# Performance work log

Measured on AMD Instinct MI355X. Metric: run time of the kernel, lower is better.

## Reference

```python
import jax, jax.numpy as jnp
import numpy as np

EPS = 1e-6

def setup_inputs() -> dict:
    key = jax.random.key(0)
    k1, k2 = jax.random.split(key)
    B, M, N, D = 4, 4096, 4096, 64
    input_features = jax.random.uniform(k1, (B, N, D), dtype=jnp.float32)
    input_associations = jax.random.uniform(k2, (B, M, N), dtype=jnp.float32)
    return {"input_features": input_features, "input_associations": input_associations}

def reference(input_features, input_associations):
    # feat: [B, N, D], assoc: [B, M, N]
    assoc_safe = input_associations + EPS
    assoc_norm = assoc_safe / jnp.sum(assoc_safe, axis=2, keepdims=True)  # normalize over N
    # weighted aggregation == batched matmul: [B,M,N] @ [B,N,D] -> [B,M,D]
    return jnp.einsum('bmn,bnd->bmd', assoc_norm, input_features)
```

## Files before the change

### kernel.cpp

```cpp
#include <hip/hip_runtime.h>

constexpr int Bn = 4;
constexpr int Mm = 4096;
constexpr int Nn = 4096;
constexpr int Dd = 64;
#define EPS_VAL 1e-6f

typedef __attribute__((ext_vector_type(8))) short short8_t;
typedef __attribute__((ext_vector_type(4))) float floatx4;

__device__ __forceinline__ unsigned short f32_to_bf16_rne(float x) {
    unsigned u = __float_as_uint(x);
    unsigned r = u + 0x7FFFu + ((u >> 16) & 1u);
    return (unsigned short)(r >> 16);
}

__global__ __launch_bounds__(256) void transpose_feat_kernel(
    const float* __restrict__ feat, unsigned short* __restrict__ ft)
{
    __shared__ unsigned short tile[64][66];
    const int b  = blockIdx.x >> 6;
    const int n0 = (blockIdx.x & 63) * 64;
    const int t  = threadIdx.x;
    const int row = t >> 2;
    const int seg = t & 3;

    const float* src = feat + ((size_t)(b * Nn + n0 + row)) * Dd + seg * 16;
    #pragma unroll
    for (int v = 0; v < 4; ++v) {
        float4 f = ((const float4*)src)[v];
        tile[row][seg * 16 + v * 4 + 0] = f32_to_bf16_rne(f.x);
        tile[row][seg * 16 + v * 4 + 1] = f32_to_bf16_rne(f.y);
        tile[row][seg * 16 + v * 4 + 2] = f32_to_bf16_rne(f.z);
        tile[row][seg * 16 + v * 4 + 3] = f32_to_bf16_rne(f.w);
    }
    __syncthreads();

    const int d    = row;
    const int nseg = seg;
    short8_t v0, v1;
    #pragma unroll
    for (int i = 0; i < 8; ++i) v0[i] = (short)tile[nseg * 16 + i][d];
    #pragma unroll
    for (int i = 0; i < 8; ++i) v1[i] = (short)tile[nseg * 16 + 8 + i][d];

    unsigned short* dst = ft + ((size_t)(b * Dd + d)) * Nn + n0 + nseg * 16;
    *(short8_t*)(dst)     = v0;
    *(short8_t*)(dst + 8) = v1;
}

__global__ __launch_bounds__(256, 1) void agg_kernel(
    const float* __restrict__ assoc, const unsigned short* __restrict__ ft,
    float* __restrict__ out)
{
    const int b  = blockIdx.x >> 6;
    const int mt = blockIdx.x & 63;
    const int w  = threadIdx.x >> 6;
    const int l  = threadIdx.x & 63;
    const int q  = l >> 4;
    const int mi = l & 15;
    const int m0 = mt * 64 + w * 16;

    const float* aptr = assoc + ((size_t)b * Mm + (size_t)(m0 + mi)) * Nn + q * 8;
    const unsigned short* fptr = ft + (size_t)b * Dd * Nn + (size_t)mi * Nn + q * 8;

    floatx4 acc0 = {0.f, 0.f, 0.f, 0.f};
    floatx4 acc1 = acc0, acc2 = acc0, acc3 = acc0;
    float s0 = 0.f, s1 = 0.f;

    #pragma unroll 4
    for (int k0 = 0; k0 < Nn; k0 += 32) {
        float4 alo = *(const float4*)(aptr + k0);
        float4 ahi = *(const float4*)(aptr + k0 + 4);
        float av[8] = {alo.x, alo.y, alo.z, alo.w, ahi.x, ahi.y, ahi.z, ahi.w};

        short8_t afrag;
        #pragma unroll
        for (int j = 0; j < 8; ++j) {
            unsigned short h = f32_to_bf16_rne(av[j] + EPS_VAL);
            afrag[j] = (short)h;
            float hv = __uint_as_float(((unsigned)h) << 16);
            if (j & 1) s1 += hv; else s0 += hv;
        }

        short8_t bf0 = *(const short8_t*)(fptr + k0);
        short8_t bf1 = *(const short8_t*)(fptr + k0 + 16 * Nn);
        short8_t bf2 = *(const short8_t*)(fptr + k0 + 32 * Nn);
        short8_t bf3 = *(const short8_t*)(fptr + k0 + 48 * Nn);

        acc0 = __builtin_amdgcn_mfma_f32_16x16x32_bf16(afrag, bf0, acc0, 0, 0, 0);
        acc1 = __builtin_amdgcn_mfma_f32_16x16x32_bf16(afrag, bf1, acc1, 0, 0, 0);
        acc2 = __builtin_amdgcn_mfma_f32_16x16x32_bf16(afrag, bf2, acc2, 0, 0, 0);
        acc3 = __builtin_amdgcn_mfma_f32_16x16x32_bf16(afrag, bf3, acc3, 0, 0, 0);
    }

    float s = s0 + s1;
    s += __shfl_xor(s, 16);
    s += __shfl_xor(s, 32);

    #pragma unroll
    for (int r = 0; r < 4; ++r) {
        float Sr  = __shfl(s, q * 4 + r);
        float inv = 1.0f / Sr;
        size_t base = ((size_t)b * Mm + (size_t)(m0 + q * 4 + r)) * Dd + mi;
        out[base +  0] = acc0[r] * inv;
        out[base + 16] = acc1[r] * inv;
        out[base + 32] = acc2[r] * inv;
        out[base + 48] = acc3[r] * inv;
    }
}

extern "C" void kernel_launch(void* const* d_in, const int* in_sizes, int n_in,
                              void* d_out, int out_size, void* d_ws, size_t ws_size,
                              hipStream_t stream) {
    const float* feat  = (const float*)d_in[0];
    const float* assoc = (const float*)d_in[1];
    float* out = (float*)d_out;
    unsigned short* ft = (unsigned short*)d_ws;

    hipLaunchKernelGGL(transpose_feat_kernel, dim3(Bn * (Nn / 64)), dim3(256), 0, stream,
                       feat, ft);
    hipLaunchKernelGGL(agg_kernel, dim3(Bn * (Mm / 64)), dim3(256), 0, stream,
                       assoc, ft, out);
}
```

Measured before the change: 382.7 us.

## Split K across waves with shared-memory reduction and quadruple block count

Result: slower. 409.6 us (+7.0%).

```diff
diff --git a/kernel.cpp b/kernel.cpp
--- a/kernel.cpp
+++ b/kernel.cpp
@@ -49,64 +49,118 @@
     *(short8_t*)(dst + 8) = v1;
 }
 
-__global__ __launch_bounds__(256, 1) void agg_kernel(
+__global__ __launch_bounds__(256, 4) void agg_kernel(
     const float* __restrict__ assoc, const unsigned short* __restrict__ ft,
     float* __restrict__ out)
 {
-    const int b  = blockIdx.x >> 6;
-    const int mt = blockIdx.x & 63;
+    const int b  = blockIdx.x >> 8;
+    const int mt = blockIdx.x & 255;
     const int w  = threadIdx.x >> 6;
     const int l  = threadIdx.x & 63;
     const int q  = l >> 4;
     const int mi = l & 15;
-    const int m0 = mt * 64 + w * 16;
+    const int m0 = mt * 16;
 
-    const float* aptr = assoc + ((size_t)b * Mm + (size_t)(m0 + mi)) * Nn + q * 8;
-    const unsigned short* fptr = ft + (size_t)b * Dd * Nn + (size_t)mi * Nn + q * 8;
+    const int kbase = w * (Nn / 4) + q * 8;
+
+    const float* aptr = assoc + ((size_t)b * Mm + (size_t)(m0 + mi)) * Nn + kbase;
+    const unsigned short* fptr = ft + (size_t)b * Dd * Nn + (size_t)mi * Nn + kbase;
 
     floatx4 acc0 = {0.f, 0.f, 0.f, 0.f};
     floatx4 acc1 = acc0, acc2 = acc0, acc3 = acc0;
     float s0 = 0.f, s1 = 0.f;
 
-    #pragma unroll 4
-    for (int k0 = 0; k0 < Nn; k0 += 32) {
-        float4 alo = *(const float4*)(aptr + k0);
-        float4 ahi = *(const float4*)(aptr + k0 + 4);
-        float av[8] = {alo.x, alo.y, alo.z, alo.w, ahi.x, ahi.y, ahi.z, ahi.w};
+    #pragma unroll 1
+    for (int k0 = 0; k0 < Nn / 4; k0 += 64) {
+        float4 a0 = *(const float4*)(aptr + k0);
+        float4 a1 = *(const float4*)(aptr + k0 + 4);
+        float4 a2 = *(const float4*)(aptr + k0 + 32);
+        float4 a3 = *(const float4*)(aptr + k0 + 36);
 
-        short8_t afrag;
-        #pragma unroll
-        for (int j = 0; j < 8; ++j) {
-            unsigned short h = f32_to_bf16_rne(av[j] + EPS_VAL);
-            afrag[j] = (short)h;
-            float hv = __uint_as_float(((unsigned)h) << 16);
-            if (j & 1) s1 += hv; else s0 += hv;
+        const unsigned short* fp = fptr + k0;
+        short8_t b00 = *(const short8_t*)(fp);
+        short8_t b01 = *(const short8_t*)(fp + 16 * Nn);
+        short8_t b02 = *(const short8_t*)(fp + 32 * Nn);
+        short8_t b03 = *(const short8_t*)(fp + 48 * Nn);
+        short8_t b10 = *(const short8_t*)(fp + 32);
+        short8_t b11 = *(const short8_t*)(fp + 32 + 16 * Nn);
+        short8_t b12 = *(const short8_t*)(fp + 32 + 32 * Nn);
+        short8_t b13 = *(const short8_t*)(fp + 32 + 48 * Nn);
+
+        short8_t af0, af1;
+        {
+            float av[8] = {a0.x, a0.y, a0.z, a0.w, a1.x, a1.y, a1.z, a1.w};
+            #pragma unroll
+            for (int j = 0; j < 8; ++j) {
+                unsigned short h = f32_to_bf16_rne(av[j] + EPS_VAL);
+                af0[j] = (short)h;
+                float hv = __uint_as_float(((unsigned)h) << 16);
+                if (j & 1) s1 += hv; else s0 += hv;
+            }
+        }
+        {
+            float av[8] = {a2.x, a2.y, a2.z, a2.w, a3.x, a3.y, a3.z, a3.w};
+            #pragma unroll
+            for (int j = 0; j < 8; ++j) {
+                unsigned short h = f32_to_bf16_rne(av[j] + EPS_VAL);
+                af1[j] = (short)h;
+                float hv = __uint_as_float(((unsigned)h) << 16);
+                if (j & 1) s1 += hv; else s0 += hv;
+            }
         }
 
-        short8_t bf0 = *(const short8_t*)(fptr + k0);
-        short8_t bf1 = *(const short8_t*)(fptr + k0 + 16 * Nn);
-        short8_t bf2 = *(const short8_t*)(fptr + k0 + 32 * Nn);
-        short8_t bf3 = *(const short8_t*)(fptr + k0 + 48 * Nn);
-
-        acc0 = __builtin_amdgcn_mfma_f32_16x16x32_bf16(afrag, bf0, acc0, 0, 0, 0);
-        acc1 = __builtin_amdgcn_mfma_f32_16x16x32_bf16(afrag, bf1, acc1, 0, 0, 0);
-        acc2 = __builtin_amdgcn_mfma_f32_16x16x32_bf16(afrag, bf2, acc2, 0, 0, 0);
-        acc3 = __builtin_amdgcn_mfma_f32_16x16x32_bf16(afrag, bf3, acc3, 0, 0, 0);
+        acc0 = __builtin_amdgcn_mfma_f32_16x16x32_bf16(af0, b00, acc0, 0, 0, 0);
+        acc1 = __builtin_amdgcn_mfma_f32_16x16x32_bf16(af0, b01, acc1, 0, 0, 0);
+        acc2 = __builtin_amdgcn_mfma_f32_16x16x32_bf16(af0, b02, acc2, 0, 0, 0);
+        acc3 = __builtin_amdgcn_mfma_f32_16x16x32_bf16(af0, b03, acc3, 0, 0, 0);
+        acc0 = __builtin_amdgcn_mfma_f32_16x16x32_bf16(af1, b10, acc0, 0, 0, 0);
+        acc1 = __builtin_amdgcn_mfma_f32_16x16x32_bf16(af1, b11, acc1, 0, 0, 0);
+        acc2 = __builtin_amdgcn_mfma_f32_16x16x32_bf16(af1, b12, acc2, 0, 0, 0);
+        acc3 = __builtin_amdgcn_mfma_f32_16x16x32_bf16(af1, b13, acc3, 0, 0, 0);
     }
 
     float s = s0 + s1;
     s += __shfl_xor(s, 16);
     s += __shfl_xor(s, 32);
 
-    #pragma unroll
-    for (int r = 0; r < 4; ++r) {
-        float Sr  = __shfl(s, q * 4 + r);
-        float inv = 1.0f / Sr;
-        size_t base = ((size_t)b * Mm + (size_t)(m0 + q * 4 + r)) * Dd + mi;
-        out[base +  0] = acc0[r] * inv;
-        out[base + 16] = acc1[r] * inv;
-        out[base + 32] = acc2[r] * inv;
-        out[base + 48] = acc3[r] * inv;
+    __shared__ float redacc[3][64][17];
+    if (w != 0) {
+        float* p = redacc[w - 1][l];
+        #pragma unroll
+        for (int i = 0; i < 4; ++i) {
+            p[i]      = acc0[i];
+            p[4 + i]  = acc1[i];
+            p[8 + i]  = acc2[i];
+            p[12 + i] = acc3[i];
+        }
+        p[16] = s;
+    }
+    __syncthreads();
+
+    if (w == 0) {
+        #pragma unroll
+        for (int ww = 0; ww < 3; ++ww) {
+            const float* p = redacc[ww][l];
+            #pragma unroll
+            for (int i = 0; i < 4; ++i) {
+                acc0[i] += p[i];
+                acc1[i] += p[4 + i];
+                acc2[i] += p[8 + i];
+                acc3[i] += p[12 + i];
+            }
+            s += p[16];
+        }
+
+        #pragma unroll
+        for (int r = 0; r < 4; ++r) {
+            float Sr  = __shfl(s, q * 4 + r);
+            float inv = 1.0f / Sr;
+            size_t base = ((size_t)b * Mm + (size_t)(m0 + q * 4 + r)) * Dd + mi;
+            out[base +  0] = acc0[r] * inv;
+            out[base + 16] = acc1[r] * inv;
+            out[base + 32] = acc2[r] * inv;
+            out[base + 48] = acc3[r] * inv;
+        }
     }
 }
 
@@ -120,6 +174,6 @@
 
     hipLaunchKernelGGL(transpose_feat_kernel, dim3(Bn * (Nn / 64)), dim3(256), 0, stream,
                        feat, ft);
-    hipLaunchKernelGGL(agg_kernel, dim3(Bn * (Mm / 64)), dim3(256), 0, stream,
+    hipLaunchKernelGGL(agg_kernel, dim3(Bn * (Mm / 16)), dim3(256), 0, stream,
                        assoc, ft, out);
 }
```

## Split the K dimension across wave pairs and reduce partial sums in shared memory

Applied to the files above, without the earlier changes.

After: 403.8 us. +5.5%, slower.

```diff
diff --git a/kernel.cpp b/kernel.cpp
--- a/kernel.cpp
+++ b/kernel.cpp
@@ -49,27 +49,31 @@
     *(short8_t*)(dst + 8) = v1;
 }
 
-__global__ __launch_bounds__(256, 1) void agg_kernel(
+__global__ __launch_bounds__(256, 2) void agg_kernel(
     const float* __restrict__ assoc, const unsigned short* __restrict__ ft,
     float* __restrict__ out)
 {
-    const int b  = blockIdx.x >> 6;
-    const int mt = blockIdx.x & 63;
+    const int b  = blockIdx.x >> 7;
+    const int mt = blockIdx.x & 127;
     const int w  = threadIdx.x >> 6;
+    const int rg = w >> 1;
+    const int nh = w & 1;
     const int l  = threadIdx.x & 63;
     const int q  = l >> 4;
     const int mi = l & 15;
-    const int m0 = mt * 64 + w * 16;
+    const int m0 = mt * 32 + rg * 16;
 
-    const float* aptr = assoc + ((size_t)b * Mm + (size_t)(m0 + mi)) * Nn + q * 8;
-    const unsigned short* fptr = ft + (size_t)b * Dd * Nn + (size_t)mi * Nn + q * 8;
+    const float* aptr = assoc + ((size_t)b * Mm + (size_t)(m0 + mi)) * Nn
+                      + nh * (Nn / 2) + q * 8;
+    const unsigned short* fptr = ft + (size_t)b * Dd * Nn + (size_t)mi * Nn
+                               + nh * (Nn / 2) + q * 8;
 
     floatx4 acc0 = {0.f, 0.f, 0.f, 0.f};
     floatx4 acc1 = acc0, acc2 = acc0, acc3 = acc0;
     float s0 = 0.f, s1 = 0.f;
 
     #pragma unroll 4
-    for (int k0 = 0; k0 < Nn; k0 += 32) {
+    for (int k0 = 0; k0 < Nn / 2; k0 += 32) {
         float4 alo = *(const float4*)(aptr + k0);
         float4 ahi = *(const float4*)(aptr + k0 + 4);
         float av[8] = {alo.x, alo.y, alo.z, alo.w, ahi.x, ahi.y, ahi.z, ahi.w};
@@ -98,15 +102,41 @@
     s += __shfl_xor(s, 16);
     s += __shfl_xor(s, 32);
 
-    #pragma unroll
-    for (int r = 0; r < 4; ++r) {
-        float Sr  = __shfl(s, q * 4 + r);
-        float inv = 1.0f / Sr;
-        size_t base = ((size_t)b * Mm + (size_t)(m0 + q * 4 + r)) * Dd + mi;
-        out[base +  0] = acc0[r] * inv;
-        out[base + 16] = acc1[r] * inv;
-        out[base + 32] = acc2[r] * inv;
-        out[base + 48] = acc3[r] * inv;
+    __shared__ float red[2][64][17];
+    if (nh == 1) {
+        float* p = red[rg][l];
+        #pragma unroll
+        for (int i = 0; i < 4; ++i) {
+            p[i]      = acc0[i];
+            p[4 + i]  = acc1[i];
+            p[8 + i]  = acc2[i];
+            p[12 + i] = acc3[i];
+        }
+        p[16] = s;
+    }
+    __syncthreads();
+
+    if (nh == 0) {
+        const float* p = red[rg][l];
+        #pragma unroll
+        for (int i = 0; i < 4; ++i) {
+            acc0[i] += p[i];
+            acc1[i] += p[4 + i];
+            acc2[i] += p[8 + i];
+            acc3[i] += p[12 + i];
+        }
+        s += p[16];
+
+        #pragma unroll
+        for (int r = 0; r < 4; ++r) {
+            float Sr  = __shfl(s, q * 4 + r);
+            float inv = 1.0f / Sr;
+            size_t base = ((size_t)b * Mm + (size_t)(m0 + q * 4 + r)) * Dd + mi;
+            out[base +  0] = acc0[r] * inv;
+            out[base + 16] = acc1[r] * inv;
+            out[base + 32] = acc2[r] * inv;
+            out[base + 48] = acc3[r] * inv;
+        }
     }
 }
 
@@ -120,6 +150,6 @@
 
     hipLaunchKernelGGL(transpose_feat_kernel, dim3(Bn * (Nn / 64)), dim3(256), 0, stream,
                        feat, ft);
-    hipLaunchKernelGGL(agg_kernel, dim3(Bn * (Mm / 64)), dim3(256), 0, stream,
+    hipLaunchKernelGGL(agg_kernel, dim3(Bn * (Mm / 32)), dim3(256), 0, stream,
                        assoc, ft, out);
 }
```
